# Performance work log

Measured on AMD Instinct MI355X. Metric: run time of the kernel, lower is better.

Reference implementation:

```python
import jax, jax.numpy as jnp
from jax import lax
import numpy as np

B, L, D = 8, 2048, 512
Q, K = 8, 2048


def setup_inputs() -> dict:
    key = jax.random.key(0)
    kx, kc = jax.random.split(key)
    x = jax.random.normal(kx, (B, L, D), dtype=jnp.float32)
    codebooks = jax.random.normal(kc, (Q, K, D), dtype=jnp.float32)  # Q stacked [K, D] embedding tables
    return {"x": x, "codebooks": codebooks}


def reference(x, codebooks):
    # Residual VQ: at each level, nearest-codeword lookup on the residual.
    # cdist argmin == squared-distance argmin: ||r||^2 - 2 r.c + ||c||^2.
    cb_sq = jnp.sum(codebooks * codebooks, axis=-1)  # [Q, K]

    def step(residual, level):
        cb, cb2 = level  # [K, D], [K]
        r2 = jnp.sum(residual * residual, axis=-1, keepdims=True)  # [B, L, 1]
        dots = jnp.einsum('bld,kd->blk', residual, cb)  # [B, L, K]
        dist2 = r2 - 2.0 * dots + cb2  # [B, L, K]
        idx = jnp.argmin(dist2, axis=-1)  # [B, L]
        quant = cb[idx]  # [B, L, D] gather
        return residual - quant, (idx, quant)

    _, (indices, quants) = lax.scan(step, x, (codebooks, cb_sq))
    quantized = jnp.sum(quants, axis=0)  # [B, L, D]
    indices = jnp.moveaxis(indices, 0, 1)  # [B, Q, L] (torch.stack(dim=1))
    return indices, quantized
```

## Files before the change

### kernel.cpp

```cpp
#include <hip/hip_runtime.h>

#define BB 8
#define LL 2048
#define DD 512
#define QQ 8
#define KK 2048
#define MM (BB*LL)

#define BMt 128
#define BNt 128
#define NSTEPS 16
#define NTILES (KK/BNt)
#define MTILES (MM/BMt)

typedef __attribute__((ext_vector_type(8))) short short8;
typedef __attribute__((ext_vector_type(4))) float f32x4;

#define GLDS(src, dst) __builtin_amdgcn_global_load_lds( \
    (const __attribute__((address_space(1))) void*)(src), \
    (__attribute__((address_space(3))) void*)(dst), 16, 0, 0)

__device__ __forceinline__ ushort f2bf(float f) {
    uint u = __float_as_uint(f);
    u += 0x7FFFu + ((u >> 16) & 1u);
    return (ushort)(u >> 16);
}

__global__ __launch_bounds__(256) void cb2_kernel(const float* __restrict__ cb,
                                                  float* __restrict__ cb2) {
    int row  = blockIdx.x * 4 + (threadIdx.x >> 6);
    int lane = threadIdx.x & 63;
    const float* r = cb + (size_t)row * DD + lane * 8;
    float4 a = *(const float4*)r;
    float4 b = *(const float4*)(r + 4);
    float s = a.x*a.x + a.y*a.y + a.z*a.z + a.w*a.w
            + b.x*b.x + b.y*b.y + b.z*b.z + b.w*b.w;
    #pragma unroll
    for (int off = 32; off >= 1; off >>= 1) s += __shfl_xor(s, off);
    if (lane == 0) cb2[row] = s;
}

__global__ __launch_bounds__(256) void bprep_kernel(const float* __restrict__ cbq,
                                                    short8* __restrict__ bh) {
    int r = blockIdx.x * 256 + threadIdx.x;
    int colr   = r & 15;
    int kk     = (r >> 4) & 3;
    int colblk = (r >> 6) & 7;
    int ks     = (r >> 9) & 15;
    int nt     = r >> 13;
    const float* src = cbq + (size_t)(nt * 128 + colblk * 16 + colr) * DD + ks * 32 + kk * 8;
    float f[8];
    *(float4*)&f[0] = *(const float4*)src;
    *(float4*)&f[4] = *(const float4*)(src + 4);
    short8 h8;
    #pragma unroll
    for (int j = 0; j < 8; j++) h8[j] = (short)f2bf(f[j]);
    bh[r] = h8;
}

__global__ __launch_bounds__(256) void aprep0_kernel(const float* __restrict__ x,
                                                     float* __restrict__ resid,
                                                     short8* __restrict__ ah) {
    const int wid  = threadIdx.x >> 6;
    const int lane = threadIdx.x & 63;
    const int row  = blockIdx.x * 4 + wid;
    const float* src = x + (size_t)row * DD + lane * 8;
    float4 v0 = *(const float4*)src;
    float4 v1 = *(const float4*)(src + 4);
    float* dst = resid + (size_t)row * DD + lane * 8;
    *(float4*)dst       = v0;
    *(float4*)(dst + 4) = v1;
    short8 h;
    h[0] = (short)f2bf(v0.x); h[1] = (short)f2bf(v0.y);
    h[2] = (short)f2bf(v0.z); h[3] = (short)f2bf(v0.w);
    h[4] = (short)f2bf(v1.x); h[5] = (short)f2bf(v1.y);
    h[6] = (short)f2bf(v1.z); h[7] = (short)f2bf(v1.w);
    ah[(size_t)row * 64 + lane] = h;
}

__global__ __launch_bounds__(256, 4) void gemm_argmin_kernel(
    const short8* __restrict__ ah,
    const short8* __restrict__ bh,
    const float*  __restrict__ cb2q,
    float*        __restrict__ blockv1,
    uint4*        __restrict__ blockmask,
    float W)
{
    __shared__ short8 smem[2][1024];

    const int id   = blockIdx.x;
    const int xcd  = id & 7;
    const int slot = id >> 3;
    const int nt   = slot & 15;
    const int mt   = xcd * 16 + (slot >> 4);

    const int t    = threadIdx.x;
    const int wid  = t >> 6;
    const int lane = t & 63;
    const int wr   = wid >> 1, wc = wid & 1;
    const int l15  = lane & 15, l4 = lane >> 4;

    f32x4 acc[4][4];
    #pragma unroll
    for (int n = 0; n < 4; n++)
        #pragma unroll
        for (int m = 0; m < 4; m++) acc[n][m] = (f32x4){0.f, 0.f, 0.f, 0.f};

    const char* aSrc = (const char*)ah + (size_t)mt * 131072;
    const char* bSrc = (const char*)bh + (size_t)nt * 131072;

    const int rlo = lane >> 2;
    const int kb  = (lane & 3) * 16;

    auto STAGE = [&](int ks, int buf) {
        char* dst = (char*)&smem[buf][0];
        const char* bs = bSrc + (size_t)ks * 8192;
        #pragma unroll
        for (int j = 0; j < 2; j++) {
            int c = wid * 2 + j;
            GLDS(aSrc + (size_t)(c * 16 + rlo) * 1024 + ks * 64 + kb,
                 dst + c * 1024 + lane * 16);
            GLDS(bs + c * 1024 + lane * 16, dst + 8192 + c * 1024);
        }
    };

    int buf = 0;
    STAGE(0, 0);

    for (int ks = 0; ks < NSTEPS; ks++) {
        __syncthreads();
        if (ks < NSTEPS - 1) STAGE(ks + 1, buf ^ 1);

        short8 af[4], bf[4];
        #pragma unroll
        for (int m = 0; m < 4; m++)
            af[m] = smem[buf][wr * 256 + m * 64 + (l15 << 2) + l4];
        #pragma unroll
        for (int n = 0; n < 4; n++)
            bf[n] = smem[buf][512 + wc * 256 + n * 64 + lane];

        #pragma unroll
        for (int n = 0; n < 4; n++)
            #pragma unroll
            for (int m = 0; m < 4; m++)
                acc[n][m] = __builtin_amdgcn_mfma_f32_16x16x32_bf16(bf[n], af[m], acc[n][m], 0, 0, 0);

        buf ^= 1;
    }

    float* halfmin = (float*)&smem[0][0];

    f32x4 c2v[4];
    #pragma unroll
    for (int n = 0; n < 4; n++)
        c2v[n] = *(const f32x4*)&cb2q[nt * 128 + wc * 64 + n * 16 + (l4 << 2)];

    #pragma unroll
    for (int m = 0; m < 4; m++) {
        float v1 = 3.4e38f;
        #pragma unroll
        for (int n = 0; n < 4; n++)
            #pragma unroll
            for (int r = 0; r < 4; r++)
                v1 = fminf(v1, fmaf(-2.f, acc[n][m][r], c2v[n][r]));
        v1 = fminf(v1, __shfl_xor(v1, 16));
        v1 = fminf(v1, __shfl_xor(v1, 32));
        if (l4 == 0) halfmin[((wr << 6) + (m << 4) + l15) * 2 + wc] = v1;
    }
    __syncthreads();

    #pragma unroll
    for (int m = 0; m < 4; m++) {
        int rowl = (wr << 6) + (m << 4) + l15;
        float vt = fminf(halfmin[rowl * 2], halfmin[rowl * 2 + 1]);
        float thrm = vt + W;
        uint blo = 0, bhi = 0;
        #pragma unroll
        for (int n = 0; n < 4; n++)
            #pragma unroll
            for (int r = 0; r < 4; r++) {
                float d = fmaf(-2.f, acc[n][m][r], c2v[n][r]);
                int bit = n * 16 + (l4 << 2) + r;
                if (d < thrm) { if (bit < 32) blo |= 1u << bit; else bhi |= 1u << (bit - 32); }
            }
        blo |= __shfl_xor(blo, 16); bhi |= __shfl_xor(bhi, 16);
        blo |= __shfl_xor(blo, 32); bhi |= __shfl_xor(bhi, 32);
        if (l4 == 0) {
            size_t o = (size_t)nt * MM + mt * BMt + rowl;
            ((uint2*)blockmask)[o * 2 + wc] = make_uint2(blo, bhi);
            if (wc == 0) blockv1[o] = vt;
        }
    }
}

__global__ __launch_bounds__(256) void crru_kernel(
    const float*  __restrict__ blockv1,
    const uint4*  __restrict__ blockmask,
    const float*  __restrict__ cbq,
    const float*  __restrict__ cb2q,
    float*        __restrict__ resid,
    float*        __restrict__ idx_out,
    short8*       __restrict__ ah,
    int q, float W)
{
    __shared__ float rs[4][DD];
    const int wid  = threadIdx.x >> 6;
    const int lane = threadIdx.x & 63;
    const int row  = blockIdx.x * 4 + wid;
    const int grp  = lane >> 4, gl = lane & 15;

    float v1 = 3.4e38f;
    uint4 mk = make_uint4(0, 0, 0, 0);
    if (lane < NTILES) {
        size_t o = (size_t)lane * MM + row;
        v1 = blockv1[o];
        mk = blockmask[o];
    }

    float* rrow = resid + (size_t)row * DD + lane * 8;
    float4 r0 = *(const float4*)rrow;
    float4 r1 = *(const float4*)(rrow + 4);
    *(float4*)&rs[wid][lane * 8]     = r0;
    *(float4*)&rs[wid][lane * 8 + 4] = r1;

    float g1 = v1;
    #pragma unroll
    for (int off = 32; off >= 1; off >>= 1) g1 = fminf(g1, __shfl_xor(g1, off));
    const float thr = g1 + W;

    unsigned long long act = __ballot((lane < NTILES) && (v1 < thr));

    float be = 3.4e38f; int bk = 0x7FFFFFFF;
    const float* rsw = rs[wid];

    auto eval4 = [&](int k0, int k1, int k2, int k3) {
        int kg = (grp == 0) ? k0 : (grp == 1) ? k1 : (grp == 2) ? k2 : k3;
        float d = 0.f;
        if (kg >= 0) {
            const float* cp = cbq + (size_t)kg * DD + gl * 32;
            const float* rp = rsw + gl * 32;
            #pragma unroll
            for (int j = 0; j < 8; j++) {
                float4 c = *(const float4*)(cp + j * 4);
                float4 r = *(const float4*)(rp + j * 4);
                d = fmaf(r.x, c.x, d); d = fmaf(r.y, c.y, d);
                d = fmaf(r.z, c.z, d); d = fmaf(r.w, c.w, d);
            }
        }
        #pragma unroll
        for (int off = 8; off >= 1; off >>= 1) d += __shfl_xor(d, off);
        #pragma unroll
        for (int g = 0; g < 4; g++) {
            float dg = __shfl(d, g * 16);
            int kg2 = (g == 0) ? k0 : (g == 1) ? k1 : (g == 2) ? k2 : k3;
            if (kg2 >= 0) {
                float e = fmaf(-2.f, dg, cb2q[kg2]);
                if (e < be || (e == be && kg2 < bk)) { be = e; bk = kg2; }
            }
        }
    };

    while (act) {
        int tile = __ffsll(act) - 1; act &= act - 1;
        uint m0 = __shfl((int)mk.x, tile), m1 = __shfl((int)mk.y, tile);
        uint m2 = __shfl((int)mk.z, tile), m3 = __shfl((int)mk.w, tile);
        unsigned long long lo = ((unsigned long long)m1 << 32) | m0;
        unsigned long long hi = ((unsigned long long)m3 << 32) | m2;
        int base = tile * 128;
        while (lo | hi) {
            int c0 = -1, c1 = -1, c2 = -1, c3 = -1;
            #define POP1(dst) \
                if (lo) { int b = __ffsll(lo) - 1; lo &= lo - 1; dst = base + b; } \
                else if (hi) { int b = __ffsll(hi) - 1; hi &= hi - 1; dst = base + 64 + b; }
            POP1(c0) POP1(c1) POP1(c2) POP1(c3)
            #undef POP1
            eval4(c0, c1, c2, c3);
        }
    }
    const int winner = bk;

    if (lane == 0) {
        int b = row >> 11, l = row & (LL - 1);
        idx_out[((size_t)b * QQ + q) * LL + l] = (float)winner;
    }

    const float* cw = cbq + (size_t)winner * DD + lane * 8;
    float4 c0 = *(const float4*)cw;
    float4 c1 = *(const float4*)(cw + 4);
    float4 n0 = make_float4(r0.x - c0.x, r0.y - c0.y, r0.z - c0.z, r0.w - c0.w);
    float4 n1 = make_float4(r1.x - c1.x, r1.y - c1.y, r1.z - c1.z, r1.w - c1.w);
    *(float4*)rrow       = n0;
    *(float4*)(rrow + 4) = n1;

    if (q < QQ - 1) {
        short8 h;
        h[0] = (short)f2bf(n0.x); h[1] = (short)f2bf(n0.y);
        h[2] = (short)f2bf(n0.z); h[3] = (short)f2bf(n0.w);
        h[4] = (short)f2bf(n1.x); h[5] = (short)f2bf(n1.y);
        h[6] = (short)f2bf(n1.z); h[7] = (short)f2bf(n1.w);
        ah[(size_t)row * 64 + lane] = h;
    }
}

__global__ __launch_bounds__(256) void final_kernel(const float* __restrict__ x,
                                                    float* __restrict__ qout) {
    size_t i = (size_t)blockIdx.x * 256 + threadIdx.x;
    float4 xv = ((const float4*)x)[i];
    float4 rv = ((float4*)qout)[i];
    ((float4*)qout)[i] = make_float4(xv.x - rv.x, xv.y - rv.y, xv.z - rv.z, xv.w - rv.w);
}

extern "C" void kernel_launch(void* const* d_in, const int* in_sizes, int n_in,
                              void* d_out, int out_size, void* d_ws, size_t ws_size,
                              hipStream_t stream) {
    (void)in_sizes; (void)n_in; (void)out_size; (void)ws_size;
    const float* x  = (const float*)d_in[0];
    const float* cb = (const float*)d_in[1];
    float* out = (float*)d_out;

    float* idx_out = out;
    float* resid   = out + (size_t)BB * QQ * LL;

    char* w = (char*)d_ws;
    float*  cb2       = (float*)(w);
    float*  blockv1   = (float*)(w + 0x10000);
    uint4*  blockmask = (uint4*)(w + 0x110000);
    short8* ah        = (short8*)(w + 0x510000);
    short8* bh        = (short8*)(w + 0x1510000);

    cb2_kernel<<<QQ * KK / 4, 256, 0, stream>>>(cb, cb2);
    aprep0_kernel<<<MM / 4, 256, 0, stream>>>(x, resid, ah);

    for (int q = 0; q < QQ; q++) {
        const float* cbq = cb + (size_t)q * KK * DD;
        const float* c2q = cb2 + (size_t)q * KK;
        const float W = 2.0f + 0.3f * q;

        bprep_kernel<<<KK * DD / 8 / 256, 256, 0, stream>>>(cbq, bh);

        gemm_argmin_kernel<<<NTILES * MTILES, 256, 0, stream>>>(ah, bh, c2q,
                                                                blockv1, blockmask, W);

        crru_kernel<<<MM / 4, 256, 0, stream>>>(blockv1, blockmask, cbq, c2q, resid,
                                                idx_out, ah, q, W);
    }

    final_kernel<<<MM * DD / 4 / 256, 256, 0, stream>>>(x, resid);
}
```

Before: 574.2 us.

## Load A fragments directly to registers and coalesce block mask/min stores

The GEMM-argmin kernel now reads the residual (A) bf16 fragments straight from global memory into registers instead of staging them through LDS. Only the codebook (B) tile stays in LDS, which halves the shared-memory footprint, and the loop is unrolled by two with explicit ping-pong buffers. The epilogue collects per-row masks in LDS and has 128 threads write one uint4 mask and one min value each, replacing scattered uint2 writes. The trade-off is that A loads become 16-byte global accesses strided across rows with more register pressure, in return for less LDS traffic and more room for occupancy.

```diff
diff --git a/kernel.cpp b/kernel.cpp
--- a/kernel.cpp
+++ b/kernel.cpp
@@ -86,7 +86,7 @@
     uint4*        __restrict__ blockmask,
     float W)
 {
-    __shared__ short8 smem[2][1024];
+    __shared__ short8 smem[2][512];
 
     const int id   = blockIdx.x;
     const int xcd  = id & 7;
@@ -106,11 +106,9 @@
         #pragma unroll
         for (int m = 0; m < 4; m++) acc[n][m] = (f32x4){0.f, 0.f, 0.f, 0.f};
 
-    const char* aSrc = (const char*)ah + (size_t)mt * 131072;
     const char* bSrc = (const char*)bh + (size_t)nt * 131072;
-
-    const int rlo = lane >> 2;
-    const int kb  = (lane & 3) * 16;
+    const char* aW = (const char*)ah
+                   + ((size_t)(mt * 128 + wr * 64 + l15) << 10) + (l4 << 4);
 
     auto STAGE = [&](int ks, int buf) {
         char* dst = (char*)&smem[buf][0];
@@ -118,37 +116,42 @@
         #pragma unroll
         for (int j = 0; j < 2; j++) {
             int c = wid * 2 + j;
-            GLDS(aSrc + (size_t)(c * 16 + rlo) * 1024 + ks * 64 + kb,
-                 dst + c * 1024 + lane * 16);
-            GLDS(bs + c * 1024 + lane * 16, dst + 8192 + c * 1024);
+            GLDS(bs + c * 1024 + lane * 16, dst + c * 1024);
         }
     };
-
-    int buf = 0;
-    STAGE(0, 0);
-
-    for (int ks = 0; ks < NSTEPS; ks++) {
-        __syncthreads();
-        if (ks < NSTEPS - 1) STAGE(ks + 1, buf ^ 1);
-
-        short8 af[4], bf[4];
+    auto LOADA = [&](short8* af, int ks) {
         #pragma unroll
         for (int m = 0; m < 4; m++)
-            af[m] = smem[buf][wr * 256 + m * 64 + (l15 << 2) + l4];
+            af[m] = *(const short8*)(aW + m * 16384 + ks * 64);
+    };
+    auto COMPUTE = [&](int buf, const short8* af) {
+        short8 bf[4];
         #pragma unroll
         for (int n = 0; n < 4; n++)
-            bf[n] = smem[buf][512 + wc * 256 + n * 64 + lane];
-
+            bf[n] = smem[buf][wc * 256 + n * 64 + lane];
         #pragma unroll
         for (int n = 0; n < 4; n++)
             #pragma unroll
             for (int m = 0; m < 4; m++)
                 acc[n][m] = __builtin_amdgcn_mfma_f32_16x16x32_bf16(bf[n], af[m], acc[n][m], 0, 0, 0);
-
-        buf ^= 1;
+    };
+
+    short8 afA[4], afB[4];
+    STAGE(0, 0);
+    LOADA(afA, 0);
+
+    for (int ks = 0; ks < NSTEPS; ks += 2) {
+        __syncthreads();
+        STAGE(ks + 1, 1);
+        LOADA(afB, ks + 1);
+        COMPUTE(0, afA);
+        __syncthreads();
+        if (ks + 2 < NSTEPS) { STAGE(ks + 2, 0); LOADA(afA, ks + 2); }
+        COMPUTE(1, afB);
     }
 
     float* halfmin = (float*)&smem[0][0];
+    uint2* maskS   = (uint2*)((char*)&smem[0][0] + 1024);
 
     f32x4 c2v[4];
     #pragma unroll
@@ -185,11 +188,16 @@
             }
         blo |= __shfl_xor(blo, 16); bhi |= __shfl_xor(bhi, 16);
         blo |= __shfl_xor(blo, 32); bhi |= __shfl_xor(bhi, 32);
-        if (l4 == 0) {
-            size_t o = (size_t)nt * MM + mt * BMt + rowl;
-            ((uint2*)blockmask)[o * 2 + wc] = make_uint2(blo, bhi);
-            if (wc == 0) blockv1[o] = vt;
-        }
+        if (l4 == 0) maskS[rowl * 2 + wc] = make_uint2(blo, bhi);
+    }
+    __syncthreads();
+
+    if (t < BMt) {
+        float vt = fminf(halfmin[t * 2], halfmin[t * 2 + 1]);
+        uint2 a = maskS[t * 2], b = maskS[t * 2 + 1];
+        size_t o = (size_t)nt * MM + mt * BMt + t;
+        blockv1[o] = vt;
+        blockmask[o] = make_uint4(a.x, a.y, b.x, b.y);
     }
 }
 
```

After: 812.6 us. +41.5%, slower.

## Enlarge GEMM tile to 256x256 with 8 waves, swizzled LDS and interleaved staging

Applied to the files above, without the earlier changes.

Rewrites the distance GEMM to use 256x256 output tiles per 512-thread block with BK=64. Both operands are now row-major bf16 and are staged into XOR-swizzled LDS with a 64KB double buffer. Global-to-LDS loads are interleaved with four MFMA phases under raised wave priority and raw s_barrier syncs. The masks and minima for each 128-column half are gathered in LDS and written out in the same per-128-column layout crru expects. The goal is higher arithmetic intensity and fewer LDS bank conflicts, at the cost of lower occupancy (128KB LDS per block) and more register pressure.

```diff
diff --git a/kernel.cpp b/kernel.cpp
--- a/kernel.cpp
+++ b/kernel.cpp
@@ -7,11 +7,7 @@
 #define KK 2048
 #define MM (BB*LL)
 
-#define BMt 128
-#define BNt 128
-#define NSTEPS 16
-#define NTILES (KK/BNt)
-#define MTILES (MM/BMt)
+#define NTILES 16
 
 typedef __attribute__((ext_vector_type(8))) short short8;
 typedef __attribute__((ext_vector_type(4))) float f32x4;
@@ -19,6 +15,9 @@
 #define GLDS(src, dst) __builtin_amdgcn_global_load_lds( \
     (const __attribute__((address_space(1))) void*)(src), \
     (__attribute__((address_space(3))) void*)(dst), 16, 0, 0)
+
+#define BARX()  asm volatile("s_barrier" ::: "memory")
+#define WAIT0() asm volatile("s_waitcnt vmcnt(0)" ::: "memory")
 
 __device__ __forceinline__ ushort f2bf(float f) {
     uint u = __float_as_uint(f);
@@ -41,21 +40,19 @@
 }
 
 __global__ __launch_bounds__(256) void bprep_kernel(const float* __restrict__ cbq,
-                                                    short8* __restrict__ bh) {
-    int r = blockIdx.x * 256 + threadIdx.x;
-    int colr   = r & 15;
-    int kk     = (r >> 4) & 3;
-    int colblk = (r >> 6) & 7;
-    int ks     = (r >> 9) & 15;
-    int nt     = r >> 13;
-    const float* src = cbq + (size_t)(nt * 128 + colblk * 16 + colr) * DD + ks * 32 + kk * 8;
-    float f[8];
-    *(float4*)&f[0] = *(const float4*)src;
-    *(float4*)&f[4] = *(const float4*)(src + 4);
-    short8 h8;
-    #pragma unroll
-    for (int j = 0; j < 8; j++) h8[j] = (short)f2bf(f[j]);
-    bh[r] = h8;
+                                                    short8* __restrict__ bh2) {
+    const int wid  = threadIdx.x >> 6;
+    const int lane = threadIdx.x & 63;
+    const int col  = blockIdx.x * 4 + wid;
+    const float* src = cbq + (size_t)col * DD + lane * 8;
+    float4 v0 = *(const float4*)src;
+    float4 v1 = *(const float4*)(src + 4);
+    short8 h;
+    h[0] = (short)f2bf(v0.x); h[1] = (short)f2bf(v0.y);
+    h[2] = (short)f2bf(v0.z); h[3] = (short)f2bf(v0.w);
+    h[4] = (short)f2bf(v1.x); h[5] = (short)f2bf(v1.y);
+    h[6] = (short)f2bf(v1.z); h[7] = (short)f2bf(v1.w);
+    bh2[(size_t)col * 64 + lane] = h;
 }
 
 __global__ __launch_bounds__(256) void aprep0_kernel(const float* __restrict__ x,
@@ -78,101 +75,125 @@
     ah[(size_t)row * 64 + lane] = h;
 }
 
-__global__ __launch_bounds__(256, 4) void gemm_argmin_kernel(
+__global__ __launch_bounds__(512, 2) void gemm_argmin_kernel(
     const short8* __restrict__ ah,
-    const short8* __restrict__ bh,
+    const short8* __restrict__ bh2,
     const float*  __restrict__ cb2q,
     float*        __restrict__ blockv1,
     uint4*        __restrict__ blockmask,
     float W)
 {
-    __shared__ short8 smem[2][1024];
-
-    const int id   = blockIdx.x;
-    const int xcd  = id & 7;
-    const int slot = id >> 3;
-    const int nt   = slot & 15;
-    const int mt   = xcd * 16 + (slot >> 4);
-
-    const int t    = threadIdx.x;
-    const int wid  = t >> 6;
-    const int lane = t & 63;
-    const int wr   = wid >> 1, wc = wid & 1;
+    __shared__ char smemc[131072];
+
+    const int id  = blockIdx.x;
+    const int xcd = id & 7;
+    const int s   = id >> 3;
+    const int nt  = s & 7;
+    const int mt  = xcd * 8 + (s >> 3);
+
+    const int tid  = threadIdx.x;
+    const int wid  = tid >> 6;
+    const int lane = tid & 63;
+    const int wr   = wid >> 2;
+    const int wcn  = wid & 3;
     const int l15  = lane & 15, l4 = lane >> 4;
 
-    f32x4 acc[4][4];
+    f32x4 acc[4][8];
     #pragma unroll
     for (int n = 0; n < 4; n++)
         #pragma unroll
-        for (int m = 0; m < 4; m++) acc[n][m] = (f32x4){0.f, 0.f, 0.f, 0.f};
-
-    const char* aSrc = (const char*)ah + (size_t)mt * 131072;
-    const char* bSrc = (const char*)bh + (size_t)nt * 131072;
-
-    const int rlo = lane >> 2;
-    const int kb  = (lane & 3) * 16;
-
-    auto STAGE = [&](int ks, int buf) {
-        char* dst = (char*)&smem[buf][0];
-        const char* bs = bSrc + (size_t)ks * 8192;
-        #pragma unroll
-        for (int j = 0; j < 2; j++) {
-            int c = wid * 2 + j;
-            GLDS(aSrc + (size_t)(c * 16 + rlo) * 1024 + ks * 64 + kb,
-                 dst + c * 1024 + lane * 16);
-            GLDS(bs + c * 1024 + lane * 16, dst + 8192 + c * 1024);
-        }
-    };
-
-    int buf = 0;
-    STAGE(0, 0);
-
-    for (int ks = 0; ks < NSTEPS; ks++) {
-        __syncthreads();
-        if (ks < NSTEPS - 1) STAGE(ks + 1, buf ^ 1);
-
-        short8 af[4], bf[4];
-        #pragma unroll
-        for (int m = 0; m < 4; m++)
-            af[m] = smem[buf][wr * 256 + m * 64 + (l15 << 2) + l4];
-        #pragma unroll
-        for (int n = 0; n < 4; n++)
-            bf[n] = smem[buf][512 + wc * 256 + n * 64 + lane];
-
-        #pragma unroll
-        for (int n = 0; n < 4; n++)
-            #pragma unroll
-            for (int m = 0; m < 4; m++)
-                acc[n][m] = __builtin_amdgcn_mfma_f32_16x16x32_bf16(bf[n], af[m], acc[n][m], 0, 0, 0);
-
-        buf ^= 1;
-    }
-
-    float* halfmin = (float*)&smem[0][0];
+        for (int m = 0; m < 8; m++) acc[n][m] = (f32x4){0.f, 0.f, 0.f, 0.f};
+
+    const char* aSrc = (const char*)ah  + ((size_t)mt << 18);
+    const char* bSrc = (const char*)bh2 + ((size_t)nt << 18);
+
+    #define STAGEQ(tt, bufn, p) do { \
+        int g_ = (p) * 512 + tid; \
+        int rL_ = g_ >> 3, st_ = g_ & 7; \
+        int k_ = st_ ^ (rL_ & 7); \
+        char* db_ = smemc + (bufn) * 65536 + ((p) * 512 + wid * 64) * 16; \
+        GLDS(aSrc + (size_t)rL_ * 1024 + (tt) * 128 + k_ * 16, db_); \
+        GLDS(bSrc + (size_t)rL_ * 1024 + (tt) * 128 + k_ * 16, db_ + 32768); \
+    } while (0)
+
+    short8 af[4][2], bf[4][2];
+
+    #define LDA(mh) do { \
+        _Pragma("unroll") for (int mm = 0; mm < 4; mm++) \
+        _Pragma("unroll") for (int ks = 0; ks < 2; ks++) { \
+            int rL_ = wr * 128 + ((mh) * 4 + mm) * 16 + l15; \
+            int c_ = ks * 4 + l4; \
+            af[mm][ks] = *(const short8*)(smemc + ab + rL_ * 128 + ((c_ ^ (rL_ & 7)) << 4)); \
+        } } while (0)
+
+    #define LDB(nh) do { \
+        _Pragma("unroll") for (int nn = 0; nn < 2; nn++) \
+        _Pragma("unroll") for (int ks = 0; ks < 2; ks++) { \
+            int cL_ = wcn * 64 + ((nh) * 2 + nn) * 16 + l15; \
+            int c_ = ks * 4 + l4; \
+            bf[(nh)*2+nn][ks] = *(const short8*)(smemc + ab + 32768 + cL_ * 128 + ((c_ ^ (cL_ & 7)) << 4)); \
+        } } while (0)
+
+    #define PH(mh, nh) do { \
+        __builtin_amdgcn_s_setprio(1); \
+        _Pragma("unroll") for (int nn = 0; nn < 2; nn++) \
+        _Pragma("unroll") for (int mm = 0; mm < 4; mm++) \
+        _Pragma("unroll") for (int ks = 0; ks < 2; ks++) \
+            acc[(nh)*2+nn][(mh)*4+mm] = __builtin_amdgcn_mfma_f32_16x16x32_bf16( \
+                bf[(nh)*2+nn][ks], af[mm][ks], acc[(nh)*2+nn][(mh)*4+mm], 0, 0, 0); \
+        __builtin_amdgcn_s_setprio(0); \
+    } while (0)
+
+    STAGEQ(0, 0, 0); STAGEQ(0, 0, 1); STAGEQ(0, 0, 2); STAGEQ(0, 0, 3);
+    WAIT0();
+    BARX();
+
+    for (int t = 0; t < 8; t++) {
+        const uint ab = (uint)(t & 1) * 65536u;
+        const int nbuf = (t & 1) ^ 1;
+        LDA(0); LDB(0);
+        if (t < 7) { STAGEQ(t + 1, nbuf, 0); STAGEQ(t + 1, nbuf, 1); }
+        PH(0, 0);
+        BARX();
+        LDB(1);
+        if (t < 7) { STAGEQ(t + 1, nbuf, 2); STAGEQ(t + 1, nbuf, 3); }
+        PH(0, 1);
+        BARX();
+        LDA(1);
+        PH(1, 0);
+        BARX();
+        PH(1, 1);
+        if (t < 7) WAIT0();
+        BARX();
+    }
+
+    float* halfmin = (float*)smemc;
+    uint2* maskS   = (uint2*)(smemc + 4096);
 
     f32x4 c2v[4];
     #pragma unroll
     for (int n = 0; n < 4; n++)
-        c2v[n] = *(const f32x4*)&cb2q[nt * 128 + wc * 64 + n * 16 + (l4 << 2)];
-
-    #pragma unroll
-    for (int m = 0; m < 4; m++) {
-        float v1 = 3.4e38f;
+        c2v[n] = *(const f32x4*)&cb2q[nt * 256 + wcn * 64 + n * 16 + (l4 << 2)];
+
+    #pragma unroll
+    for (int m = 0; m < 8; m++) {
+        float v = 3.4e38f;
         #pragma unroll
         for (int n = 0; n < 4; n++)
             #pragma unroll
             for (int r = 0; r < 4; r++)
-                v1 = fminf(v1, fmaf(-2.f, acc[n][m][r], c2v[n][r]));
-        v1 = fminf(v1, __shfl_xor(v1, 16));
-        v1 = fminf(v1, __shfl_xor(v1, 32));
-        if (l4 == 0) halfmin[((wr << 6) + (m << 4) + l15) * 2 + wc] = v1;
+                v = fminf(v, fmaf(-2.f, acc[n][m][r], c2v[n][r]));
+        v = fminf(v, __shfl_xor(v, 16));
+        v = fminf(v, __shfl_xor(v, 32));
+        if (l4 == 0) halfmin[(wr * 128 + m * 16 + l15) * 4 + wcn] = v;
     }
     __syncthreads();
 
     #pragma unroll
-    for (int m = 0; m < 4; m++) {
-        int rowl = (wr << 6) + (m << 4) + l15;
-        float vt = fminf(halfmin[rowl * 2], halfmin[rowl * 2 + 1]);
+    for (int m = 0; m < 8; m++) {
+        int rL = wr * 128 + m * 16 + l15;
+        int pb = wcn & 2;
+        float vt = fminf(halfmin[rL * 4 + pb], halfmin[rL * 4 + pb + 1]);
         float thrm = vt + W;
         uint blo = 0, bhi = 0;
         #pragma unroll
@@ -185,12 +206,22 @@
             }
         blo |= __shfl_xor(blo, 16); bhi |= __shfl_xor(bhi, 16);
         blo |= __shfl_xor(blo, 32); bhi |= __shfl_xor(bhi, 32);
-        if (l4 == 0) {
-            size_t o = (size_t)nt * MM + mt * BMt + rowl;
-            ((uint2*)blockmask)[o * 2 + wc] = make_uint2(blo, bhi);
-            if (wc == 0) blockv1[o] = vt;
-        }
-    }
+        if (l4 == 0) maskS[rL * 4 + wcn] = make_uint2(blo, bhi);
+    }
+    __syncthreads();
+
+    {
+        int T = tid >> 8, rL = tid & 255;
+        float vt = fminf(halfmin[rL * 4 + T * 2], halfmin[rL * 4 + T * 2 + 1]);
+        uint2 lo = maskS[rL * 4 + T * 2], hi = maskS[rL * 4 + T * 2 + 1];
+        size_t o = (size_t)(nt * 2 + T) * MM + mt * 256 + rL;
+        blockv1[o] = vt;
+        blockmask[o] = make_uint4(lo.x, lo.y, hi.x, hi.y);
+    }
+    #undef STAGEQ
+    #undef LDA
+    #undef LDB
+    #undef PH
 }
 
 __global__ __launch_bounds__(256) void crru_kernel(
@@ -326,7 +357,7 @@
     float*  blockv1   = (float*)(w + 0x10000);
     uint4*  blockmask = (uint4*)(w + 0x110000);
     short8* ah        = (short8*)(w + 0x510000);
-    short8* bh        = (short8*)(w + 0x1510000);
+    short8* bh2       = (short8*)(w + 0x1510000);
 
     cb2_kernel<<<QQ * KK / 4, 256, 0, stream>>>(cb, cb2);
     aprep0_kernel<<<MM / 4, 256, 0, stream>>>(x, resid, ah);
@@ -336,10 +367,10 @@
         const float* c2q = cb2 + (size_t)q * KK;
         const float W = 2.0f + 0.3f * q;
 
-        bprep_kernel<<<KK * DD / 8 / 256, 256, 0, stream>>>(cbq, bh);
-
-        gemm_argmin_kernel<<<NTILES * MTILES, 256, 0, stream>>>(ah, bh, c2q,
-                                                                blockv1, blockmask, W);
+        bprep_kernel<<<KK / 4, 256, 0, stream>>>(cbq, bh2);
+
+        gemm_argmin_kernel<<<512, 512, 0, stream>>>(ah, bh2, c2q,
+                                                    blockv1, blockmask, W);
 
         crru_kernel<<<MM / 4, 256, 0, stream>>>(blockv1, blockmask, cbq, c2q, resid,
                                                 idx_out, ah, q, W);
```

New measurement: 523.4 us. 1.1x faster.
